# Performance work log

Measured on AMD Instinct MI355X. Metric: run time of the kernel, lower is better.

## Reference

```python
import jax, jax.numpy as jnp
import numpy as np

B, N, M, D = 4, 512, 512, 128
H, DOUT = 256, 128

def setup_inputs() -> dict:
    key = jax.random.key(0)
    k = jax.random.split(key, 4)
    X = jax.random.normal(k[0], (B, N, D), dtype=jnp.float32)
    Y = jax.random.normal(k[1], (B, M, D), dtype=jnp.float32)
    W1 = jax.random.normal(k[2], (2 * D, H), dtype=jnp.float32) / np.sqrt(2 * D)
    b1 = jnp.zeros((H,), dtype=jnp.float32)
    W2 = jax.random.normal(k[3], (H, DOUT), dtype=jnp.float32) / np.sqrt(H)
    b2 = jnp.zeros((DOUT,), dtype=jnp.float32)
    return {"X": X, "Y": Y, "W1": W1, "b1": b1, "W2": W2, "b2": b2}

def reference(X, Y, W1, b1, W2, b2):
    # pairs[b,n,m,:] = concat(Y[b,m], X[b,n])  -> [B,N,M,2D]
    n_ = X.shape[1]
    m_ = Y.shape[1]
    Ye = jnp.broadcast_to(Y[:, None, :, :], (X.shape[0], n_, m_, Y.shape[-1]))
    Xe = jnp.broadcast_to(X[:, :, None, :], (X.shape[0], n_, m_, X.shape[-1]))
    pairs = jnp.concatenate([Ye, Xe], axis=-1)
    # pointwise MLP: Linear -> ReLU -> Linear
    hdn = jax.nn.relu(jnp.einsum('bnmd,dh->bnmh', pairs, W1) + b1)
    Z = jnp.einsum('bnmh,ho->bnmo', hdn, W2) + b2
    # pool='sum' over the M (neighbor) dimension
    return jnp.sum(Z, axis=2)  # [B, N, DOUT]
```

## Files before the change

kernel.cpp:

```cpp
#include <hip/hip_runtime.h>

#define BB    4
#define NN    512
#define MM    512
#define DD    128
#define HH    256
#define DOUTC 128
#define NTILE 8
#define MSPLIT 4

typedef float v2f __attribute__((ext_vector_type(2)));

__global__ __launch_bounds__(256) void precompute_ac(
    const float* __restrict__ X, const float* __restrict__ Y,
    const float* __restrict__ W1, const float* __restrict__ b1,
    float* __restrict__ AC)
{
    __shared__ __align__(16) float rows[8][DD];
    const int bid = blockIdx.x;
    const int isC = bid >> 8;
    const int r0  = (bid & 255) * 8;
    const int t   = threadIdx.x;

    const float* src = isC ? X : Y;
    const float4* s4 = reinterpret_cast<const float4*>(src + (size_t)r0 * DD);
    reinterpret_cast<float4*>(&rows[0][0])[t] = s4[t];
    __syncthreads();

    const int h = t;
    float acc[8];
#pragma unroll
    for (int r = 0; r < 8; ++r) acc[r] = 0.f;

    const float* wp = W1 + (isC ? DD * HH : 0) + h;
#pragma unroll 2
    for (int d = 0; d < DD; d += 4) {
        const float w0 = wp[(d + 0) * HH];
        const float w1v = wp[(d + 1) * HH];
        const float w2v = wp[(d + 2) * HH];
        const float w3v = wp[(d + 3) * HH];
#pragma unroll
        for (int r = 0; r < 8; ++r) {
            const float4 rv = *reinterpret_cast<const float4*>(&rows[r][d]);
            acc[r] = fmaf(rv.x, w0, acc[r]);
            acc[r] = fmaf(rv.y, w1v, acc[r]);
            acc[r] = fmaf(rv.z, w2v, acc[r]);
            acc[r] = fmaf(rv.w, w3v, acc[r]);
        }
    }

    const float bias = isC ? b1[h] : 0.f;
#pragma unroll
    for (int r = 0; r < 8; ++r) {
        AC[((size_t)(isC * 2048 + r0 + r)) * HH + h] = acc[r] + bias;
    }
}

__global__ __launch_bounds__(256) void relu_sum(
    const float* __restrict__ A, const float* __restrict__ C,
    float* __restrict__ part)
{
    const int bid = blockIdx.x;
    const int ms = bid & (MSPLIT - 1);
    const int nt = (bid >> 2) & 63;
    const int b  = bid >> 8;
    const int t  = threadIdx.x;
    const int hp = t & 127;
    const int h0 = hp * 2;
    const int nh = t >> 7;
    const int n0 = nt * NTILE + nh * 4;

    v2f c[4], acc[4];
#pragma unroll
    for (int i = 0; i < 4; ++i) {
        c[i] = *reinterpret_cast<const v2f*>(&C[((size_t)(b * NN + n0 + i)) * HH + h0]);
        acc[i] = (v2f){0.f, 0.f};
    }

    const float* Ab = A + ((size_t)(b * MM + ms * (MM / MSPLIT))) * HH + h0;
#pragma unroll 4
    for (int m = 0; m < MM / MSPLIT; ++m) {
        const v2f a2 = *reinterpret_cast<const v2f*>(&Ab[(size_t)m * HH]);
#pragma unroll
        for (int i = 0; i < 4; ++i) {
            v2f s = a2 + c[i];
            s.x = fmaxf(s.x, 0.f);
            s.y = fmaxf(s.y, 0.f);
            acc[i] += s;
        }
    }

#pragma unroll
    for (int i = 0; i < 4; ++i)
        *reinterpret_cast<v2f*>(
            &part[(((size_t)(b * NN + n0 + i)) * MSPLIT + ms) * HH + h0]) = acc[i];
}

__global__ __launch_bounds__(256) void finalize(
    const float* __restrict__ part, const float* __restrict__ W2,
    const float* __restrict__ b2, float* __restrict__ out)
{
    __shared__ __align__(16) float S[8][HH];
    const int bn0 = blockIdx.x * 8;
    const int t   = threadIdx.x;

#pragma unroll
    for (int r = 0; r < 8; ++r) {
        float s = 0.f;
#pragma unroll
        for (int ms = 0; ms < MSPLIT; ++ms)
            s += part[((size_t)(bn0 + r) * MSPLIT + ms) * HH + t];
        S[r][t] = s;
    }
    __syncthreads();

    const int o     = t & 127;
    const int rbase = (t >> 7) * 4;

    float acc[4];
    const float binit = b2[o] * (float)MM;
#pragma unroll
    for (int j = 0; j < 4; ++j) acc[j] = binit;

    const float* w2p = W2 + o;
#pragma unroll 2
    for (int k = 0; k < HH; k += 4) {
        const float w0 = w2p[(k + 0) * DOUTC];
        const float w1v = w2p[(k + 1) * DOUTC];
        const float w2v = w2p[(k + 2) * DOUTC];
        const float w3v = w2p[(k + 3) * DOUTC];
#pragma unroll
        for (int j = 0; j < 4; ++j) {
            const float4 sv = *reinterpret_cast<const float4*>(&S[rbase + j][k]);
            acc[j] = fmaf(sv.x, w0, acc[j]);
            acc[j] = fmaf(sv.y, w1v, acc[j]);
            acc[j] = fmaf(sv.z, w2v, acc[j]);
            acc[j] = fmaf(sv.w, w3v, acc[j]);
        }
    }

#pragma unroll
    for (int j = 0; j < 4; ++j)
        out[(size_t)(bn0 + rbase + j) * DOUTC + o] = acc[j];
}

extern "C" void kernel_launch(void* const* d_in, const int* in_sizes, int n_in,
                              void* d_out, int out_size, void* d_ws, size_t ws_size,
                              hipStream_t stream) {
    const float* X  = (const float*)d_in[0];
    const float* Y  = (const float*)d_in[1];
    const float* W1 = (const float*)d_in[2];
    const float* b1 = (const float*)d_in[3];
    const float* W2 = (const float*)d_in[4];
    const float* b2 = (const float*)d_in[5];
    float* out = (float*)d_out;

    float* AC   = (float*)d_ws;
    float* A    = AC;
    float* C    = AC + 2048 * HH;
    float* part = AC + 4096 * HH;

    hipLaunchKernelGGL(precompute_ac, dim3(512), dim3(256), 0, stream,
                       X, Y, W1, b1, AC);
    hipLaunchKernelGGL(relu_sum, dim3(BB * (NN / NTILE) * MSPLIT), dim3(256), 0, stream,
                       A, C, part);
    hipLaunchKernelGGL(finalize, dim3(BB * NN / 8), dim3(256), 0, stream,
                       part, W2, b2, out);
}
```

Before: 51.11 us.

## Rewrite ReLU sum via abs identity and restructure precompute and finalize kernels

Uses relu(x) = (x + |x|)/2, so the pairwise reduction accumulates only |A+C|. Each pair then costs an add plus an add with an abs modifier instead of add, max and add. The sum of A over M and the M·C term are computed separately, and the finalize kernel combines them. The precompute kernel drops its shared-memory staging and reads input rows directly, and the finalize kernel uses 4-row tiles with paired-output vector weight loads. The trade-off is an extra serial SA reduction in a few blocks, and the abs modifier may not fold into packed FP32 ops.

```diff
diff --git a/kernel.cpp b/kernel.cpp
--- a/kernel.cpp
+++ b/kernel.cpp
@@ -6,8 +6,8 @@
 #define DD    128
 #define HH    256
 #define DOUTC 128
-#define NTILE 8
 #define MSPLIT 4
+#define MCHUNK (MM / MSPLIT)
 
 typedef float v2f __attribute__((ext_vector_type(2)));
 
@@ -16,59 +16,43 @@
     const float* __restrict__ W1, const float* __restrict__ b1,
     float* __restrict__ AC)
 {
-    __shared__ __align__(16) float rows[8][DD];
     const int bid = blockIdx.x;
     const int isC = bid >> 8;
     const int r0  = (bid & 255) * 8;
-    const int t   = threadIdx.x;
+    const int h   = threadIdx.x;
 
     const float* src = isC ? X : Y;
-    const float4* s4 = reinterpret_cast<const float4*>(src + (size_t)r0 * DD);
-    reinterpret_cast<float4*>(&rows[0][0])[t] = s4[t];
-    __syncthreads();
+    const float* row = src + (size_t)r0 * DD;
+    const float* wp  = W1 + (isC ? DD * HH : 0) + h;
 
-    const int h = t;
-    float acc[8];
+    float acc[8] = {0.f, 0.f, 0.f, 0.f, 0.f, 0.f, 0.f, 0.f};
+
+#pragma unroll 4
+    for (int d = 0; d < DD; ++d) {
+        const float w = wp[d * HH];
 #pragma unroll
-    for (int r = 0; r < 8; ++r) acc[r] = 0.f;
-
-    const float* wp = W1 + (isC ? DD * HH : 0) + h;
-#pragma unroll 2
-    for (int d = 0; d < DD; d += 4) {
-        const float w0 = wp[(d + 0) * HH];
-        const float w1v = wp[(d + 1) * HH];
-        const float w2v = wp[(d + 2) * HH];
-        const float w3v = wp[(d + 3) * HH];
-#pragma unroll
-        for (int r = 0; r < 8; ++r) {
-            const float4 rv = *reinterpret_cast<const float4*>(&rows[r][d]);
-            acc[r] = fmaf(rv.x, w0, acc[r]);
-            acc[r] = fmaf(rv.y, w1v, acc[r]);
-            acc[r] = fmaf(rv.z, w2v, acc[r]);
-            acc[r] = fmaf(rv.w, w3v, acc[r]);
-        }
+        for (int r = 0; r < 8; ++r)
+            acc[r] = fmaf(row[r * DD + d], w, acc[r]);
     }
 
     const float bias = isC ? b1[h] : 0.f;
 #pragma unroll
-    for (int r = 0; r < 8; ++r) {
+    for (int r = 0; r < 8; ++r)
         AC[((size_t)(isC * 2048 + r0 + r)) * HH + h] = acc[r] + bias;
-    }
 }
 
-__global__ __launch_bounds__(256) void relu_sum(
+__global__ __launch_bounds__(256) void abs_sum(
     const float* __restrict__ A, const float* __restrict__ C,
-    float* __restrict__ part)
+    float* __restrict__ part, float* __restrict__ SAbuf)
 {
     const int bid = blockIdx.x;
     const int ms = bid & (MSPLIT - 1);
     const int nt = (bid >> 2) & 63;
     const int b  = bid >> 8;
     const int t  = threadIdx.x;
-    const int hp = t & 127;
-    const int h0 = hp * 2;
+    const int h0 = (t & 127) * 2;
     const int nh = t >> 7;
-    const int n0 = nt * NTILE + nh * 4;
+    const int n0 = nt * 8 + nh * 4;
 
     v2f c[4], acc[4];
 #pragma unroll
@@ -77,16 +61,15 @@
         acc[i] = (v2f){0.f, 0.f};
     }
 
-    const float* Ab = A + ((size_t)(b * MM + ms * (MM / MSPLIT))) * HH + h0;
+    const float* Ab = A + ((size_t)(b * MM + ms * MCHUNK)) * HH + h0;
 #pragma unroll 4
-    for (int m = 0; m < MM / MSPLIT; ++m) {
+    for (int m = 0; m < MCHUNK; ++m) {
         const v2f a2 = *reinterpret_cast<const v2f*>(&Ab[(size_t)m * HH]);
 #pragma unroll
         for (int i = 0; i < 4; ++i) {
-            v2f s = a2 + c[i];
-            s.x = fmaxf(s.x, 0.f);
-            s.y = fmaxf(s.y, 0.f);
-            acc[i] += s;
+            const v2f s = a2 + c[i];
+            acc[i].x += fabsf(s.x);
+            acc[i].y += fabsf(s.y);
         }
     }
 
@@ -94,54 +77,58 @@
     for (int i = 0; i < 4; ++i)
         *reinterpret_cast<v2f*>(
             &part[(((size_t)(b * NN + n0 + i)) * MSPLIT + ms) * HH + h0]) = acc[i];
+
+    if (nt == 0 && nh == 0) {
+        v2f sa = (v2f){0.f, 0.f};
+#pragma unroll 4
+        for (int m = 0; m < MCHUNK; ++m)
+            sa += *reinterpret_cast<const v2f*>(&Ab[(size_t)m * HH]);
+        *reinterpret_cast<v2f*>(&SAbuf[((size_t)(b * MSPLIT + ms)) * HH + h0]) = sa;
+    }
 }
 
 __global__ __launch_bounds__(256) void finalize(
-    const float* __restrict__ part, const float* __restrict__ W2,
+    const float* __restrict__ part, const float* __restrict__ SAbuf,
+    const float* __restrict__ C, const float* __restrict__ W2,
     const float* __restrict__ b2, float* __restrict__ out)
 {
-    __shared__ __align__(16) float S[8][HH];
-    const int bn0 = blockIdx.x * 8;
+    __shared__ __align__(16) float S[4][HH];
+    const int bn0 = blockIdx.x * 4;
+    const int b   = bn0 >> 9;
     const int t   = threadIdx.x;
 
+    float sat = 0.f;
 #pragma unroll
-    for (int r = 0; r < 8; ++r) {
-        float s = 0.f;
+    for (int ms = 0; ms < MSPLIT; ++ms)
+        sat += SAbuf[((size_t)(b * MSPLIT + ms)) * HH + t];
+
+#pragma unroll
+    for (int r = 0; r < 4; ++r) {
+        float ab = 0.f;
 #pragma unroll
         for (int ms = 0; ms < MSPLIT; ++ms)
-            s += part[((size_t)(bn0 + r) * MSPLIT + ms) * HH + t];
-        S[r][t] = s;
+            ab += part[((size_t)(bn0 + r) * MSPLIT + ms) * HH + t];
+        S[r][t] = 0.5f * (sat + 512.f * C[(size_t)(bn0 + r) * HH + t] + ab);
     }
     __syncthreads();
 
-    const int o     = t & 127;
-    const int rbase = (t >> 7) * 4;
+    const int o0 = (t & 63) * 2;
+    const int r  = t >> 6;
 
-    float acc[4];
-    const float binit = b2[o] * (float)MM;
-#pragma unroll
-    for (int j = 0; j < 4; ++j) acc[j] = binit;
+    const float bi = b2[o0] * 512.f;
+    const float bj = b2[o0 + 1] * 512.f;
+    v2f acc2 = (v2f){bi, bj};
 
-    const float* w2p = W2 + o;
-#pragma unroll 2
-    for (int k = 0; k < HH; k += 4) {
-        const float w0 = w2p[(k + 0) * DOUTC];
-        const float w1v = w2p[(k + 1) * DOUTC];
-        const float w2v = w2p[(k + 2) * DOUTC];
-        const float w3v = w2p[(k + 3) * DOUTC];
-#pragma unroll
-        for (int j = 0; j < 4; ++j) {
-            const float4 sv = *reinterpret_cast<const float4*>(&S[rbase + j][k]);
-            acc[j] = fmaf(sv.x, w0, acc[j]);
-            acc[j] = fmaf(sv.y, w1v, acc[j]);
-            acc[j] = fmaf(sv.z, w2v, acc[j]);
-            acc[j] = fmaf(sv.w, w3v, acc[j]);
-        }
+    const float* w2p = W2 + o0;
+#pragma unroll 4
+    for (int k = 0; k < HH; ++k) {
+        const v2f w2v = *reinterpret_cast<const v2f*>(&w2p[k * DOUTC]);
+        const float sv = S[r][k];
+        acc2.x = fmaf(sv, w2v.x, acc2.x);
+        acc2.y = fmaf(sv, w2v.y, acc2.y);
     }
 
-#pragma unroll
-    for (int j = 0; j < 4; ++j)
-        out[(size_t)(bn0 + rbase + j) * DOUTC + o] = acc[j];
+    *reinterpret_cast<v2f*>(&out[(size_t)(bn0 + r) * DOUTC + o0]) = acc2;
 }
 
 extern "C" void kernel_launch(void* const* d_in, const int* in_sizes, int n_in,
@@ -155,15 +142,16 @@
     const float* b2 = (const float*)d_in[5];
     float* out = (float*)d_out;
 
-    float* AC   = (float*)d_ws;
-    float* A    = AC;
-    float* C    = AC + 2048 * HH;
-    float* part = AC + 4096 * HH;
+    float* AC    = (float*)d_ws;
+    float* A     = AC;
+    float* C     = AC + 2048 * HH;
+    float* part  = AC + 4096 * HH;
+    float* SAbuf = part + (size_t)BB * NN * MSPLIT * HH;
 
     hipLaunchKernelGGL(precompute_ac, dim3(512), dim3(256), 0, stream,
                        X, Y, W1, b1, AC);
-    hipLaunchKernelGGL(relu_sum, dim3(BB * (NN / NTILE) * MSPLIT), dim3(256), 0, stream,
-                       A, C, part);
-    hipLaunchKernelGGL(finalize, dim3(BB * NN / 8), dim3(256), 0, stream,
-                       part, W2, b2, out);
+    hipLaunchKernelGGL(abs_sum, dim3(BB * 64 * MSPLIT), dim3(256), 0, stream,
+                       A, C, part, SAbuf);
+    hipLaunchKernelGGL(finalize, dim3(BB * NN / 4), dim3(256), 0, stream,
+                       part, SAbuf, C, W2, b2, out);
 }
```

Result: slower. 65.81 us (+28.8%).
